# Kernel optimization log

Measured on AMD Instinct MI355X. Metric: run time of the kernel, lower is better.

Reference implementation:

```python
import jax, jax.numpy as jnp
import numpy as np

B, N, D_MODEL, H, D_K, D_V = 2, 2048, 1024, 16, 64, 64


def setup_inputs() -> dict:
    key = jax.random.key(0)
    ks = jax.random.split(key, 8)
    queries = jax.random.normal(ks[0], (B, N, D_MODEL), dtype=jnp.float32)
    keys = jax.random.normal(ks[1], (B, N, D_MODEL), dtype=jnp.float32)
    values = jax.random.normal(ks[2], (B, N, D_MODEL), dtype=jnp.float32)
    # nn.Linear weights: (out_features, in_features); init.normal_(std=0.001) in the
    # original, but we use a larger scale for a numerically meaningful test.
    Wq = jax.random.normal(ks[3], (H * D_K, D_MODEL), dtype=jnp.float32) * 0.02
    Wk = jax.random.normal(ks[4], (H * D_K, D_MODEL), dtype=jnp.float32) * 0.02
    Wv = jax.random.normal(ks[5], (H * D_V, D_MODEL), dtype=jnp.float32) * 0.02
    Wo = jax.random.normal(ks[6], (D_MODEL, H * D_V), dtype=jnp.float32) * 0.02
    bo = jnp.zeros((D_MODEL,), dtype=jnp.float32)
    return {"queries": queries, "keys": keys, "values": values,
            "Wq": Wq, "Wk": Wk, "Wv": Wv, "Wo": Wo, "bo": bo}


def reference(queries, keys, values, Wq, Wk, Wv, Wo, bo):
    b, nq, _ = queries.shape
    nk = keys.shape[1]
    scale = 1.0 / np.sqrt(D_K).astype(np.float32)
    # projections: (b, n, h, d)
    q = (queries @ Wq.T).reshape(b, nq, H, D_K)
    k = (keys @ Wk.T).reshape(b, nk, H, D_K)
    v = (values @ Wv.T).reshape(b, nk, H, D_V)
    # scaled dot-product attention; seq_mask=None, attention_weights=None, dropout p=0
    att = jnp.einsum('bqhd,bkhd->bhqk', q, k) * scale  # (b, h, nq, nk)
    att = jax.nn.softmax(att, axis=-1)
    out = jnp.einsum('bhqk,bkhd->bqhd', att, v).reshape(b, nq, H * D_V)
    return queries + (out @ Wo.T + bo)
```

## Files before the change

### kernel.cpp

```cpp
#include <hip/hip_runtime.h>
#include <hip/hip_bf16.h>
#include <stdint.h>

#define BATCH  2
#define SEQ    2048
#define DMODEL 1024
#define NHEAD  16
#define DHEAD  64

typedef unsigned short u16;
typedef __attribute__((ext_vector_type(8))) short bf16x8;
typedef __attribute__((ext_vector_type(4))) float f32x4;

__device__ __forceinline__ u16 f2bf(float x) {
    union { float f; uint32_t u; } v; v.f = x;
    uint32_t r = v.u + 0x7fffu + ((v.u >> 16) & 1u);
    return (u16)(r >> 16);
}

__device__ __forceinline__ uint32_t pk2bf(float a, float b) {
    __hip_bfloat162 h = __float22bfloat162_rn(make_float2(a, b));
    return *(uint32_t*)&h;
}

__device__ __forceinline__ float exp2_raw(float x) {
    float r;
    asm("v_exp_f32 %0, %1" : "=v"(r) : "v"(x));
    return r;
}

__device__ __forceinline__ void gload_lds16(const void* g, void* l) {
    __builtin_amdgcn_global_load_lds(
        (const __attribute__((address_space(1))) uint32_t*)(uintptr_t)g,
        (__attribute__((address_space(3))) uint32_t*)(uintptr_t)l,
        16, 0, 0);
}

__device__ __forceinline__ f32x4 mfma16(bf16x8 a, bf16x8 b, f32x4 c) {
    return __builtin_amdgcn_mfma_f32_16x16x32_bf16(a, b, c, 0, 0, 0);
}

__global__ __launch_bounds__(256) void cvt4_kernel(
    const float* s0, const float* s1, const float* s2, const float* s3,
    u16* d0, u16* d1, u16* d2, u16* d3)
{
    const float* s; u16* d;
    switch (blockIdx.y) {
        case 0: s = s0; d = d0; break;
        case 1: s = s1; d = d1; break;
        case 2: s = s2; d = d2; break;
        default: s = s3; d = d3; break;
    }
    size_t i = ((size_t)blockIdx.x * 256 + threadIdx.x) * 8;
    float4 a = *(const float4*)(s + i);
    float4 b = *(const float4*)(s + i + 4);
    union { uint4 v; u16 e[8]; } u;
    u.e[0] = f2bf(a.x); u.e[1] = f2bf(a.y); u.e[2] = f2bf(a.z); u.e[3] = f2bf(a.w);
    u.e[4] = f2bf(b.x); u.e[5] = f2bf(b.y); u.e[6] = f2bf(b.z); u.e[7] = f2bf(b.w);
    *(uint4*)(d + i) = u.v;
}

__device__ __forceinline__ void gemm_core_128_f32A(
    const float* __restrict__ A, const u16* __restrict__ Bm, int K,
    int brow, int bcol, u16* As, u16* Bs, f32x4 (&acc)[4][4])
{
    const int tid  = threadIdx.x;
    const int lane = tid & 63;
    const int wr   = ((tid >> 6) >> 1) * 64;
    const int wc   = ((tid >> 6) & 1) * 64;
    const int srow = tid >> 2;
    const int scol = (tid & 3) * 8;
    const int fr   = lane & 15;
    const int fk   = (lane >> 4) * 8;

    const float* s0 = A + (size_t)(brow + srow) * K + scol;
    const float* s1 = A + (size_t)(brow + 64 + srow) * K + scol;

    float4 a0 = *(const float4*)(s0);
    float4 a1 = *(const float4*)(s0 + 4);
    float4 b0 = *(const float4*)(s1);
    float4 b1 = *(const float4*)(s1 + 4);

    for (int k0 = 0; k0 < K; k0 += 32) {
        uint4 wA, wB;
        wA.x = pk2bf(a0.x, a0.y); wA.y = pk2bf(a0.z, a0.w);
        wA.z = pk2bf(a1.x, a1.y); wA.w = pk2bf(a1.z, a1.w);
        wB.x = pk2bf(b0.x, b0.y); wB.y = pk2bf(b0.z, b0.w);
        wB.z = pk2bf(b1.x, b1.y); wB.w = pk2bf(b1.z, b1.w);
        *(uint4*)(As + srow * 32 + scol) = wA;
        *(uint4*)(As + (64 + srow) * 32 + scol) = wB;
        gload_lds16(Bm + (size_t)(bcol + srow) * K + k0 + scol,       Bs + srow * 32 + scol);
        gload_lds16(Bm + (size_t)(bcol + 64 + srow) * K + k0 + scol,  Bs + (64 + srow) * 32 + scol);
        __builtin_amdgcn_sched_barrier(0);
        if (k0 + 32 < K) {
            a0 = *(const float4*)(s0 + k0 + 32);
            a1 = *(const float4*)(s0 + k0 + 36);
            b0 = *(const float4*)(s1 + k0 + 32);
            b1 = *(const float4*)(s1 + k0 + 36);
            asm volatile("s_waitcnt lgkmcnt(0)" ::: "memory");
            asm volatile("s_waitcnt vmcnt(4)" ::: "memory");
        } else {
            asm volatile("s_waitcnt lgkmcnt(0)" ::: "memory");
            asm volatile("s_waitcnt vmcnt(0)" ::: "memory");
        }
        __builtin_amdgcn_s_barrier();
        __builtin_amdgcn_sched_barrier(0);

        bf16x8 af[4], bfv[4];
        #pragma unroll
        for (int i = 0; i < 4; ++i) {
            af[i]  = *(const bf16x8*)(As + (wr + i * 16 + fr) * 32 + fk);
            bfv[i] = *(const bf16x8*)(Bs + (wc + i * 16 + fr) * 32 + fk);
        }
        #pragma unroll
        for (int am = 0; am < 4; ++am)
            #pragma unroll
            for (int bn = 0; bn < 4; ++bn)
                acc[am][bn] = mfma16(af[am], bfv[bn], acc[am][bn]);
        __builtin_amdgcn_s_barrier();
    }
}

__device__ __forceinline__ void gemm_core_64x128(
    const u16* __restrict__ A, const u16* __restrict__ Bm, int K,
    int brow, int bcol, u16* As, u16* Bs, f32x4 (&acc)[4][2])
{
    const int tid  = threadIdx.x;
    const int lane = tid & 63;
    const int wc   = (tid >> 6) * 32;
    const int srow = tid >> 2;
    const int scol = (tid & 3) * 8;
    const int fr   = lane & 15;
    const int fk   = (lane >> 4) * 8;

    for (int k0 = 0; k0 < K; k0 += 32) {
        gload_lds16(A  + (size_t)(brow + srow) * K + k0 + scol,       As + srow * 32 + scol);
        gload_lds16(Bm + (size_t)(bcol + srow) * K + k0 + scol,       Bs + srow * 32 + scol);
        gload_lds16(Bm + (size_t)(bcol + 64 + srow) * K + k0 + scol,  Bs + (64 + srow) * 32 + scol);
        __syncthreads();
        bf16x8 af[4], bfv[2];
        #pragma unroll
        for (int i = 0; i < 4; ++i)
            af[i]  = *(const bf16x8*)(As + (i * 16 + fr) * 32 + fk);
        #pragma unroll
        for (int i = 0; i < 2; ++i)
            bfv[i] = *(const bf16x8*)(Bs + (wc + i * 16 + fr) * 32 + fk);
        #pragma unroll
        for (int am = 0; am < 4; ++am)
            #pragma unroll
            for (int bn = 0; bn < 2; ++bn)
                acc[am][bn] = mfma16(af[am], bfv[bn], acc[am][bn]);
        __syncthreads();
    }
}

__global__ __launch_bounds__(256) void gemm_qkv_kernel(
    const float* __restrict__ Xq, const float* __restrict__ Xk, const float* __restrict__ Xv,
    const u16* __restrict__ Wq, const u16* __restrict__ Wk, const u16* __restrict__ Wv,
    u16* __restrict__ Qo, u16* __restrict__ Ko, u16* __restrict__ Vt,
    int M, int Nn, int K)
{
    __shared__ u16 As[128 * 32];
    __shared__ u16 Bs[128 * 32];
    const int z = blockIdx.z;
    const float* A = (z == 0) ? Xq : (z == 1) ? Xk : Xv;
    const u16* Bm  = (z == 0) ? Wq : (z == 1) ? Wk : Wv;
    const float scale = (z == 0) ? 0.18033688011112042f : 1.0f;

    const int lin  = blockIdx.y * gridDim.x + blockIdx.x;
    const int nlin = (lin & 7) * 32 + (lin >> 3);
    const int brow = (nlin >> 3) * 128;
    const int bcol = (nlin & 7) * 128;
    f32x4 acc[4][4];
    #pragma unroll
    for (int am = 0; am < 4; ++am)
        #pragma unroll
        for (int bn = 0; bn < 4; ++bn)
            acc[am][bn] = (f32x4){0.f, 0.f, 0.f, 0.f};

    gemm_core_128_f32A(A, Bm, K, brow, bcol, As, Bs, acc);

    const int lane = threadIdx.x & 63;
    const int wr = ((threadIdx.x >> 6) >> 1) * 64;
    const int wc = ((threadIdx.x >> 6) & 1) * 64;
    const int fr = lane & 15;
    const int fj4 = (lane >> 4) * 4;

    if (z == 2) {
        #pragma unroll
        for (int am = 0; am < 4; ++am)
            #pragma unroll
            for (int bn = 0; bn < 4; ++bn) {
                int row = brow + wr + am * 16 + fj4;
                int col = bcol + wc + bn * 16 + fr;
                int b   = row >> 11;
                int n   = row & 2047;
                int h   = col >> 6;
                int d   = col & 63;
                uint2 w;
                w.x = pk2bf(acc[am][bn][0], acc[am][bn][1]);
                w.y = pk2bf(acc[am][bn][2], acc[am][bn][3]);
                *(uint2*)(Vt + ((size_t)(b * 16 + h) * DHEAD + d) * SEQ + n) = w;
            }
    } else {
        u16* D = (z == 0) ? Qo : Ko;
        #pragma unroll
        for (int am = 0; am < 4; ++am)
            #pragma unroll
            for (int bn = 0; bn < 4; ++bn)
                #pragma unroll
                for (int j = 0; j < 4; ++j) {
                    int row = brow + wr + am * 16 + fj4 + j;
                    int col = bcol + wc + bn * 16 + fr;
                    D[(size_t)row * Nn + col] = f2bf(acc[am][bn][j] * scale);
                }
    }
}

__global__ __launch_bounds__(256, 2) void gemm_out_kernel(
    const u16* __restrict__ A, const u16* __restrict__ Bm,
    const float* __restrict__ bias, const float* __restrict__ resid,
    float* __restrict__ D, int M, int Nn, int K)
{
    __shared__ u16 As[64 * 32];
    __shared__ u16 Bs[128 * 32];

    const int lin  = blockIdx.y * gridDim.x + blockIdx.x;
    const int nlin = (lin & 7) * 64 + (lin >> 3);
    const int brow = (nlin >> 3) * 64;
    const int bcol = (nlin & 7) * 128;
    f32x4 acc[4][2];
    #pragma unroll
    for (int am = 0; am < 4; ++am)
        #pragma unroll
        for (int bn = 0; bn < 2; ++bn)
            acc[am][bn] = (f32x4){0.f, 0.f, 0.f, 0.f};

    gemm_core_64x128(A, Bm, K, brow, bcol, As, Bs, acc);

    const int lane = threadIdx.x & 63;
    const int wc = (threadIdx.x >> 6) * 32;
    const int fr = lane & 15;
    const int fj4 = (lane >> 4) * 4;
    #pragma unroll
    for (int am = 0; am < 4; ++am)
        #pragma unroll
        for (int bn = 0; bn < 2; ++bn)
            #pragma unroll
            for (int j = 0; j < 4; ++j) {
                int row = brow + am * 16 + fj4 + j;
                int col = bcol + wc + bn * 16 + fr;
                D[(size_t)row * Nn + col] = acc[am][bn][j] + bias[col] + resid[(size_t)row * Nn + col];
            }
}

__global__ __launch_bounds__(1024, 1) void attn_kernel(
    const u16* __restrict__ Qb, const u16* __restrict__ Kb, const u16* __restrict__ Vt,
    u16* __restrict__ AO)
{
    __shared__ u16 Ks[3][64 * 64];
    __shared__ u16 Vs[3][64 * 64];
    __shared__ u16 Ps[256 * 72];

    const int tid  = threadIdx.x;
    const int lane = tid & 63;
    const int wave = tid >> 6;

    const int lin  = blockIdx.x;
    const int nlin = (lin & 7) * 32 + (lin >> 3);
    const int qblk = nlin & 7;
    const int bh   = nlin >> 3;

    const size_t rowbase = (size_t)(bh >> 4) * SEQ;
    const int colbase = (bh & 15) * DHEAD;
    const int q0 = qblk * 256;
    const int fr  = lane & 15;
    const int g   = lane >> 4;
    const int fk  = g * 8;
    const int fj4 = g * 4;
    const int qw  = wave * 16;

    const u16* Kh = Kb + rowbase * DMODEL + colbase;
    const u16* Vh = Vt + (size_t)bh * DHEAD * SEQ;

    const int st  = tid & 511;
    const int sr  = st >> 3;
    const int sc  = st & 7;
    const int scs = (sc ^ (sr & 7)) << 3;
    const int sdst = sr * 64 + sc * 8;
    const bool stageK = (tid < 512);

    bf16x8 qf[2];
    #pragma unroll
    for (int kc = 0; kc < 2; ++kc)
        qf[kc] = *(const bf16x8*)(Qb + (rowbase + q0 + qw + fr) * DMODEL
                                     + colbase + kc * 32 + fk);

    f32x4 oacc[4];
    float lsum = 0.f;
    #pragma unroll
    for (int dn = 0; dn < 4; ++dn) oacc[dn] = (f32x4){0.f, 0.f, 0.f, 0.f};

    if (stageK) {
        gload_lds16(Kh + (size_t)sr * DMODEL + scs,        &Ks[0][sdst]);
        gload_lds16(Kh + (size_t)(64 + sr) * DMODEL + scs, &Ks[1][sdst]);
    } else {
        gload_lds16(Vh + (size_t)sr * SEQ + scs,           &Vs[0][sdst]);
        gload_lds16(Vh + (size_t)sr * SEQ + 64 + scs,      &Vs[1][sdst]);
    }

    const int NT = SEQ / 64;
    int cur = 0;
    for (int t = 0; t < NT; ++t) {
        if (t < NT - 1) {
            asm volatile("s_waitcnt vmcnt(1)" ::: "memory");
        } else {
            asm volatile("s_waitcnt vmcnt(0)" ::: "memory");
        }
        __builtin_amdgcn_s_barrier();
        __builtin_amdgcn_sched_barrier(0);

        if (t + 2 < NT) {
            int wbuf = cur + 2; if (wbuf >= 3) wbuf -= 3;
            const size_t kvn = (size_t)(t + 2) * 64;
            if (stageK) gload_lds16(Kh + (kvn + sr) * DMODEL + scs,    &Ks[wbuf][sdst]);
            else        gload_lds16(Vh + (size_t)sr * SEQ + kvn + scs, &Vs[wbuf][sdst]);
        }

        const u16* K0 = &Ks[cur][0];
        const u16* V0 = &Vs[cur][0];

        f32x4 sacc[4];
        #pragma unroll
        for (int bn = 0; bn < 4; ++bn) sacc[bn] = (f32x4){0.f, 0.f, 0.f, 0.f};
        __builtin_amdgcn_s_setprio(1);
        #pragma unroll
        for (int bn = 0; bn < 4; ++bn) {
            bf16x8 kf0 = *(const bf16x8*)(K0 + (bn * 16 + fr) * 64 + (((g)     ^ (fr & 7)) << 3));
            bf16x8 kf1 = *(const bf16x8*)(K0 + (bn * 16 + fr) * 64 + (((4 + g) ^ (fr & 7)) << 3));
            sacc[bn] = mfma16(kf0, qf[0], sacc[bn]);
            sacc[bn] = mfma16(kf1, qf[1], sacc[bn]);
        }
        __builtin_amdgcn_s_setprio(0);

        {
            float lacc = 0.f;
            #pragma unroll
            for (int bn = 0; bn < 4; ++bn) {
                float p0 = exp2_raw(sacc[bn][0]);
                float p1 = exp2_raw(sacc[bn][1]);
                float p2 = exp2_raw(sacc[bn][2]);
                float p3 = exp2_raw(sacc[bn][3]);
                uint2 w;
                w.x = pk2bf(p0, p1);
                w.y = pk2bf(p2, p3);
                *(uint2*)(Ps + (qw + fr) * 72 + bn * 16 + fj4) = w;
                lacc += (p0 + p1) + (p2 + p3);
            }
            lsum += lacc;
        }

        bf16x8 pf[2];
        #pragma unroll
        for (int kc = 0; kc < 2; ++kc)
            pf[kc] = *(const bf16x8*)(Ps + (qw + fr) * 72 + kc * 32 + fk);
        __builtin_amdgcn_s_setprio(1);
        #pragma unroll
        for (int dn = 0; dn < 4; ++dn) {
            bf16x8 vf0 = *(const bf16x8*)(V0 + (dn * 16 + fr) * 64 + (((g)     ^ (fr & 7)) << 3));
            bf16x8 vf1 = *(const bf16x8*)(V0 + (dn * 16 + fr) * 64 + (((4 + g) ^ (fr & 7)) << 3));
            oacc[dn] = mfma16(pf[0], vf0, oacc[dn]);
            oacc[dn] = mfma16(pf[1], vf1, oacc[dn]);
        }
        __builtin_amdgcn_s_setprio(0);

        cur = (cur == 2) ? 0 : cur + 1;
    }

    float invj[4];
    {
        float l = lsum;
        l += __shfl_xor(l, 16);
        l += __shfl_xor(l, 32);
        #pragma unroll
        for (int j = 0; j < 4; ++j) {
            float lj = __shfl(l, (lane & 48) | (fj4 + j));
            invj[j] = 1.f / lj;
        }
    }

    #pragma unroll
    for (int dn = 0; dn < 4; ++dn)
        #pragma unroll
        for (int j = 0; j < 4; ++j) {
            int row = q0 + qw + fj4 + j;
            AO[(rowbase + row) * DMODEL + colbase + dn * 16 + fr] =
                f2bf(oacc[dn][j] * invj[j]);
        }
}

extern "C" void kernel_launch(void* const* d_in, const int* in_sizes, int n_in,
                              void* d_out, int out_size, void* d_ws, size_t ws_size,
                              hipStream_t stream)
{
    const float* q_f  = (const float*)d_in[0];
    const float* k_f  = (const float*)d_in[1];
    const float* v_f  = (const float*)d_in[2];
    const float* Wq_f = (const float*)d_in[3];
    const float* Wk_f = (const float*)d_in[4];
    const float* Wv_f = (const float*)d_in[5];
    const float* Wo_f = (const float*)d_in[6];
    const float* bo_f = (const float*)d_in[7];

    char* ws = (char*)d_ws;
    const size_t ACT = (size_t)BATCH * SEQ * DMODEL * sizeof(u16);
    const size_t WSZ = (size_t)DMODEL * DMODEL * sizeof(u16);
    u16* Wqb = (u16*)(ws);
    u16* Wkb = (u16*)(ws + WSZ);
    u16* Wvb = (u16*)(ws + 2 * WSZ);
    u16* Wob = (u16*)(ws + 3 * WSZ);
    u16* Qb  = (u16*)(ws + 4 * WSZ);
    u16* Kb  = (u16*)(ws + 4 * WSZ + ACT);
    u16* Vt  = (u16*)(ws + 4 * WSZ + 2 * ACT);
    u16* AO  = (u16*)(ws + 4 * WSZ + 3 * ACT);

    const int M = BATCH * SEQ;
    const int Nn = DMODEL;
    const int K = DMODEL;

    cvt4_kernel<<<dim3(512, 4, 1), 256, 0, stream>>>(
        Wq_f, Wk_f, Wv_f, Wo_f, Wqb, Wkb, Wvb, Wob);

    gemm_qkv_kernel<<<dim3(Nn / 128, M / 128, 3), 256, 0, stream>>>(
        q_f, k_f, v_f, Wqb, Wkb, Wvb, Qb, Kb, Vt, M, Nn, K);

    attn_kernel<<<dim3(256, 1, 1), 1024, 0, stream>>>(Qb, Kb, Vt, AO);

    gemm_out_kernel<<<dim3(Nn / 128, M / 64, 1), 256, 0, stream>>>(
        AO, Wob, bo_f, q_f, (float*)d_out, M, Nn, K);
}
```

Before: 112.7 us.

## Double-buffer LDS tiles in QKV projection GEMM to overlap loads with MFMA

The QKV projection GEMM core now uses two LDS buffers for the A and B tiles. The next tile's bf16-converted A data and async B loads are written into the alternate buffer while MFMAs run on the current one, which removes one barrier per K-step. It also raises wave priority around the MFMA block with s_setprio. LDS use doubles to 32 KB per block, which may lower occupancy, and the waitcnt placement has to stay correct for the overlapping loads.

Result: no change. 112.4 us (-0.3%).

```diff
diff --git a/kernel.cpp b/kernel.cpp
--- a/kernel.cpp
+++ b/kernel.cpp
@@ -60,9 +60,10 @@
     *(uint4*)(d + i) = u.v;
 }
 
-__device__ __forceinline__ void gemm_core_128_f32A(
+__device__ __forceinline__ void gemm_core_128_f32A_dbuf(
     const float* __restrict__ A, const u16* __restrict__ Bm, int K,
-    int brow, int bcol, u16* As, u16* Bs, f32x4 (&acc)[4][4])
+    int brow, int bcol, u16 (&As)[2][128 * 32], u16 (&Bs)[2][128 * 32],
+    f32x4 (&acc)[4][4])
 {
     const int tid  = threadIdx.x;
     const int lane = tid & 63;
@@ -75,49 +76,79 @@
 
     const float* s0 = A + (size_t)(brow + srow) * K + scol;
     const float* s1 = A + (size_t)(brow + 64 + srow) * K + scol;
+    const int NT = K / 32;
 
     float4 a0 = *(const float4*)(s0);
     float4 a1 = *(const float4*)(s0 + 4);
     float4 b0 = *(const float4*)(s1);
     float4 b1 = *(const float4*)(s1 + 4);
-
-    for (int k0 = 0; k0 < K; k0 += 32) {
+    {
         uint4 wA, wB;
         wA.x = pk2bf(a0.x, a0.y); wA.y = pk2bf(a0.z, a0.w);
         wA.z = pk2bf(a1.x, a1.y); wA.w = pk2bf(a1.z, a1.w);
         wB.x = pk2bf(b0.x, b0.y); wB.y = pk2bf(b0.z, b0.w);
         wB.z = pk2bf(b1.x, b1.y); wB.w = pk2bf(b1.z, b1.w);
-        *(uint4*)(As + srow * 32 + scol) = wA;
-        *(uint4*)(As + (64 + srow) * 32 + scol) = wB;
-        gload_lds16(Bm + (size_t)(bcol + srow) * K + k0 + scol,       Bs + srow * 32 + scol);
-        gload_lds16(Bm + (size_t)(bcol + 64 + srow) * K + k0 + scol,  Bs + (64 + srow) * 32 + scol);
-        __builtin_amdgcn_sched_barrier(0);
-        if (k0 + 32 < K) {
-            a0 = *(const float4*)(s0 + k0 + 32);
-            a1 = *(const float4*)(s0 + k0 + 36);
-            b0 = *(const float4*)(s1 + k0 + 32);
-            b1 = *(const float4*)(s1 + k0 + 36);
-            asm volatile("s_waitcnt lgkmcnt(0)" ::: "memory");
-            asm volatile("s_waitcnt vmcnt(4)" ::: "memory");
-        } else {
-            asm volatile("s_waitcnt lgkmcnt(0)" ::: "memory");
-            asm volatile("s_waitcnt vmcnt(0)" ::: "memory");
-        }
-        __builtin_amdgcn_s_barrier();
-        __builtin_amdgcn_sched_barrier(0);
+        *(uint4*)(&As[0][srow * 32 + scol]) = wA;
+        *(uint4*)(&As[0][(64 + srow) * 32 + scol]) = wB;
+    }
+    gload_lds16(Bm + (size_t)(bcol + srow) * K + scol,      &Bs[0][srow * 32 + scol]);
+    gload_lds16(Bm + (size_t)(bcol + 64 + srow) * K + scol, &Bs[0][(64 + srow) * 32 + scol]);
+    __builtin_amdgcn_sched_barrier(0);
+    a0 = *(const float4*)(s0 + 32);
+    a1 = *(const float4*)(s0 + 36);
+    b0 = *(const float4*)(s1 + 32);
+    b1 = *(const float4*)(s1 + 36);
+    asm volatile("s_waitcnt lgkmcnt(0)" ::: "memory");
+    asm volatile("s_waitcnt vmcnt(4)" ::: "memory");
+    __builtin_amdgcn_s_barrier();
+    __builtin_amdgcn_sched_barrier(0);
+
+    for (int t = 0; t < NT; ++t) {
+        const int cb = t & 1;
+        if (t + 1 < NT) {
+            uint4 wA, wB;
+            wA.x = pk2bf(a0.x, a0.y); wA.y = pk2bf(a0.z, a0.w);
+            wA.z = pk2bf(a1.x, a1.y); wA.w = pk2bf(a1.z, a1.w);
+            wB.x = pk2bf(b0.x, b0.y); wB.y = pk2bf(b0.z, b0.w);
+            wB.z = pk2bf(b1.x, b1.y); wB.w = pk2bf(b1.z, b1.w);
+            *(uint4*)(&As[cb ^ 1][srow * 32 + scol]) = wA;
+            *(uint4*)(&As[cb ^ 1][(64 + srow) * 32 + scol]) = wB;
+            const int kn = (t + 1) * 32;
+            gload_lds16(Bm + (size_t)(bcol + srow) * K + kn + scol,      &Bs[cb ^ 1][srow * 32 + scol]);
+            gload_lds16(Bm + (size_t)(bcol + 64 + srow) * K + kn + scol, &Bs[cb ^ 1][(64 + srow) * 32 + scol]);
+            __builtin_amdgcn_sched_barrier(0);
+            if (t + 2 < NT) {
+                a0 = *(const float4*)(s0 + (t + 2) * 32);
+                a1 = *(const float4*)(s0 + (t + 2) * 32 + 4);
+                b0 = *(const float4*)(s1 + (t + 2) * 32);
+                b1 = *(const float4*)(s1 + (t + 2) * 32 + 4);
+            }
+        }
 
         bf16x8 af[4], bfv[4];
         #pragma unroll
         for (int i = 0; i < 4; ++i) {
-            af[i]  = *(const bf16x8*)(As + (wr + i * 16 + fr) * 32 + fk);
-            bfv[i] = *(const bf16x8*)(Bs + (wc + i * 16 + fr) * 32 + fk);
-        }
+            af[i]  = *(const bf16x8*)(&As[cb][(wr + i * 16 + fr) * 32 + fk]);
+            bfv[i] = *(const bf16x8*)(&Bs[cb][(wc + i * 16 + fr) * 32 + fk]);
+        }
+        __builtin_amdgcn_s_setprio(1);
         #pragma unroll
         for (int am = 0; am < 4; ++am)
             #pragma unroll
             for (int bn = 0; bn < 4; ++bn)
                 acc[am][bn] = mfma16(af[am], bfv[bn], acc[am][bn]);
-        __builtin_amdgcn_s_barrier();
+        __builtin_amdgcn_s_setprio(0);
+
+        if (t + 1 < NT) {
+            asm volatile("s_waitcnt lgkmcnt(0)" ::: "memory");
+            if (t + 2 < NT) {
+                asm volatile("s_waitcnt vmcnt(4)" ::: "memory");
+            } else {
+                asm volatile("s_waitcnt vmcnt(0)" ::: "memory");
+            }
+            __builtin_amdgcn_s_barrier();
+            __builtin_amdgcn_sched_barrier(0);
+        }
     }
 }
 
@@ -160,8 +191,8 @@
     u16* __restrict__ Qo, u16* __restrict__ Ko, u16* __restrict__ Vt,
     int M, int Nn, int K)
 {
-    __shared__ u16 As[128 * 32];
-    __shared__ u16 Bs[128 * 32];
+    __shared__ u16 As[2][128 * 32];
+    __shared__ u16 Bs[2][128 * 32];
     const int z = blockIdx.z;
     const float* A = (z == 0) ? Xq : (z == 1) ? Xk : Xv;
     const u16* Bm  = (z == 0) ? Wq : (z == 1) ? Wk : Wv;
@@ -178,7 +209,7 @@
         for (int bn = 0; bn < 4; ++bn)
             acc[am][bn] = (f32x4){0.f, 0.f, 0.f, 0.f};
 
-    gemm_core_128_f32A(A, Bm, K, brow, bcol, As, Bs, acc);
+    gemm_core_128_f32A_dbuf(A, Bm, K, brow, bcol, As, Bs, acc);
 
     const int lane = threadIdx.x & 63;
     const int wr = ((threadIdx.x >> 6) >> 1) * 64;
```
